# Kernel optimization log

Measured on AMD Instinct MI355X. Metric: run time of the kernel, lower is better.

The kernel has to match this reference:

```python
import jax, jax.numpy as jnp
import numpy as np
import math

B, C, T0, Q0 = 2, 48, 250, 65
H = 192; KS = 4; HS = 1; NH = 4; E = 8; F = 65; DV = 12; HID2 = 384
EPS = 1e-5


def ln_clamp(x, g, b, axes, eps=EPS):
    # LayerNormalization4D / 4DCF: std = sqrt(clamp(var, eps))
    mu = x.mean(axis=axes, keepdims=True)
    var = x.var(axis=axes, keepdims=True)
    return (x - mu) / jnp.sqrt(jnp.maximum(var, eps)) * g + b


def torch_ln(x, g, b, eps=EPS):
    # torch.nn.LayerNorm over last dim: sqrt(var + eps)
    mu = x.mean(axis=-1, keepdims=True)
    var = x.var(axis=-1, keepdims=True)
    return (x - mu) / jnp.sqrt(var + eps) * g + b


def mha(x, in_w, in_b, out_w, out_b, nh):
    # torch.nn.MultiheadAttention, batch_first, self-attention
    N, L, Cm = x.shape
    qkv = x @ in_w.T + in_b
    q, k, v = jnp.split(qkv, 3, axis=-1)
    dh = Cm // nh
    hd = lambda t: t.reshape(N, L, nh, dh).transpose(0, 2, 1, 3)
    q, k, v = hd(q), hd(k), hd(v)
    att = jax.nn.softmax(jnp.einsum('nhld,nhmd->nhlm', q, k) / jnp.sqrt(jnp.float32(dh)), axis=-1)
    o = jnp.einsum('nhlm,nhmd->nhld', att, v).transpose(0, 2, 1, 3).reshape(N, L, Cm)
    return o @ out_w.T + out_b


def lstm_dir(x, wi, wh, bi, bh, reverse=False):
    # x: [N, L, D]; torch gate order i,f,g,o
    Hd = wh.shape[1]
    xs = jnp.swapaxes(x, 0, 1)
    if reverse:
        xs = xs[::-1]
    pre = jnp.einsum('lnd,gd->lng', xs, wi) + bi + bh  # [L,N,4H]

    def step(carry, p):
        hprev, cprev = carry
        gates = p + hprev @ wh.T
        i, f, g, o = jnp.split(gates, 4, axis=-1)
        c = jax.nn.sigmoid(f) * cprev + jax.nn.sigmoid(i) * jnp.tanh(g)
        hnew = jax.nn.sigmoid(o) * jnp.tanh(c)
        return (hnew, c), hnew

    h0 = jnp.zeros((x.shape[0], Hd), x.dtype)
    _, ys = jax.lax.scan(step, (h0, h0), pre)
    if reverse:
        ys = ys[::-1]
    return jnp.swapaxes(ys, 0, 1)


def bilstm(x, wif, whf, bif, bhf, wib, whb, bib, bhb):
    return jnp.concatenate([lstm_dir(x, wif, whf, bif, bhf, False),
                            lstm_dir(x, wib, whb, bib, bhb, True)], axis=-1)


def unfold1d(x, ks, hs):
    # x: [N, C, Q] -> [N, L, C*ks], channel-major like F.unfold
    N, Cc, Qq = x.shape
    L = (Qq - ks) // hs + 1
    cols = jnp.stack([x[:, :, k:k + (L - 1) * hs + 1:hs] for k in range(ks)], axis=-1)  # [N,C,L,ks]
    return cols.transpose(0, 2, 1, 3).reshape(N, L, Cc * ks)


def conv_transpose1d(x, w, b, stride):
    # x: [N, Cin, L], w: [Cin, Cout, ks] (torch ConvTranspose1d layout); overlap-add
    N, Ci, L = x.shape
    ks = w.shape[2]
    out_len = (L - 1) * stride + ks
    y = jnp.einsum('nil,iok->nolk', x, w)
    out = jnp.zeros((N, w.shape[1], out_len), x.dtype)
    for k in range(ks):
        out = out.at[:, :, k:k + (L - 1) * stride + 1:stride].add(y[..., k])
    return out + b[:, None]


def _forward(x, af_in_w, af_in_b, af_out_w, af_out_b, naf_g, naf_b, at_in_w, at_in_b, at_out_w, at_out_b, nat_g, nat_b, intra_ng, intra_nb, inter_ng, inter_nb, intra_wif, intra_whf, intra_bif, intra_bhf, intra_wib, intra_whb, intra_bib, intra_bhb, inter_wif, inter_whf, inter_bif, inter_bhf, inter_wib, inter_whb, inter_bib, inter_bhb, il_w, il_b, itl_w, itl_b, qw, qb, qa, qg, qbt, kw, kb, ka, kg, kbt, vw, vb, va, vg, vbt, pw, pb, pa, pg, pbt, fin_w, fin_b, fdw_w, fdw_b, fout_w, fout_b):
    Bb, Cc, old_T, old_Q = x.shape
    T = math.ceil((old_T - KS) / HS) * HS + KS
    Qd = math.ceil((old_Q - KS) / HS) * HS + KS
    x = jnp.pad(x, ((0, 0), (0, 0), (0, T - old_T), (0, Qd - old_Q)))
    input_ = x

    # ---- intra (frequency) path ----
    z = ln_clamp(input_, intra_ng[None, :, None, None], intra_nb[None, :, None, None], (1,))
    seq = z.transpose(0, 2, 3, 1).reshape(Bb * T, Qd, Cc)  # [B*T, Q, C]
    att = mha(seq, af_in_w, af_in_b, af_out_w, af_out_b, NH)
    seq = torch_ln(att + seq, naf_g, naf_b)
    u = unfold1d(seq.transpose(0, 2, 1), KS, HS)
    r = bilstm(u, intra_wif, intra_whf, intra_bif, intra_bhf, intra_wib, intra_whb, intra_bib, intra_bhb)
    r = conv_transpose1d(r.transpose(0, 2, 1), il_w, il_b, HS)  # [B*T, C, Qd]
    intra = r.reshape(Bb, T, Cc, Qd).transpose(0, 2, 1, 3) + input_
    input_ = intra

    # ---- inter (time) path ----
    z = ln_clamp(input_, inter_ng[None, :, None, None], inter_nb[None, :, None, None], (1,))
    seq = z.transpose(0, 3, 2, 1).reshape(Bb * Qd, T, Cc)  # [B*Q, T, C]
    att = mha(seq, at_in_w, at_in_b, at_out_w, at_out_b, NH)
    seq = torch_ln(att + seq, nat_g, nat_b)
    u = unfold1d(seq.transpose(0, 2, 1), KS, HS)
    r = bilstm(u, inter_wif, inter_whf, inter_bif, inter_bhf, inter_wib, inter_whb, inter_bib, inter_bhb)
    r = conv_transpose1d(r.transpose(0, 2, 1), itl_w, itl_b, HS)  # [B*Qd, C, T]
    inter = r.reshape(Bb, Qd, Cc, T).transpose(0, 2, 3, 1) + input_
    inter = inter[:, :, :old_T, :old_Q]

    # ---- custom per-head conv attention ----
    bt = inter  # [B, C, t, f]

    def head_proj(w, bias, a, g, beta):
        y = jnp.einsum('bctf,hec->hbetf', bt, w) + bias[:, None, :, None, None]
        y = jnp.where(y >= 0, y, a[:, None, None, None, None] * y)  # PReLU per head
        return ln_clamp(y, g[:, None, :, None, :], beta[:, None, :, None, :], (2, 4))

    Qh = head_proj(qw, qb, qa, qg, qbt)  # [h,B,E,t,f]
    Kh = head_proj(kw, kb, ka, kg, kbt)
    Vh = head_proj(vw, vb, va, vg, vbt)  # [h,B,dv,t,f]
    h_, _, E_, t_, f_ = Qh.shape
    dv = Vh.shape[2]
    Qf = Qh.transpose(0, 1, 3, 2, 4).reshape(h_, Bb, t_, E_ * f_)
    Kf = Kh.transpose(0, 1, 3, 2, 4).reshape(h_, Bb, t_, E_ * f_)
    Vf = Vh.transpose(0, 1, 3, 2, 4).reshape(h_, Bb, t_, dv * f_)
    attm = jax.nn.softmax(jnp.einsum('hbtd,hbsd->hbts', Qf, Kf) / jnp.sqrt(jnp.float32(E_ * f_)), axis=-1)
    Vo = jnp.einsum('hbts,hbsd->hbtd', attm, Vf).reshape(h_, Bb, t_, dv, f_)
    Vo = Vo.transpose(1, 0, 3, 2, 4).reshape(Bb, h_ * dv, t_, f_)  # head-major channel concat
    pj = jnp.einsum('bctf,oc->botf', Vo, pw) + pb[None, :, None, None]
    pj = jnp.where(pj >= 0, pj, pa * pj)
    pj = ln_clamp(pj, pg[None, :, None, :], pbt[None, :, None, :], (1, 3))
    out = pj + inter

    # ---- gated-dconv FFN ----
    pi = jnp.einsum('bctf,oc->botf', out, fin_w) + fin_b[None, :, None, None]
    dwc = jax.lax.conv_general_dilated(pi, fdw_w, (1, 1), ((1, 1), (1, 1)),
                                       dimension_numbers=('NCHW', 'OIHW', 'NCHW'),
                                       feature_group_count=fdw_w.shape[0]) + fdw_b[None, :, None, None]
    x1, x2 = jnp.split(dwc, 2, axis=1)
    ffn = jnp.einsum('bctf,oc->botf', jax.nn.gelu(x1, approximate=False) * x2, fout_w) + fout_b[None, :, None, None]
    return ffn + out


def setup_inputs() -> dict:
    key = jax.random.key(0)
    cnt = [0]

    def rn(shape, s=0.05):
        cnt[0] += 1
        return jax.random.normal(jax.random.fold_in(key, cnt[0]), shape, dtype=jnp.float32) * s

    z = lambda *s: jnp.zeros(s, jnp.float32)
    o = lambda *s: jnp.ones(s, jnp.float32)
    d = {}
    d['x'] = rn((B, C, T0, Q0), 1.0)
    for p in ['af', 'at']:
        d[p + '_in_w'] = rn((3 * C, C)); d[p + '_in_b'] = z(3 * C)
        d[p + '_out_w'] = rn((C, C)); d[p + '_out_b'] = z(C)
    d['naf_g'] = o(C); d['naf_b'] = z(C); d['nat_g'] = o(C); d['nat_b'] = z(C)
    d['intra_ng'] = o(C); d['intra_nb'] = z(C); d['inter_ng'] = o(C); d['inter_nb'] = z(C)
    for p in ['intra', 'inter']:
        for s in ['f', 'b']:
            d[p + '_wi' + s] = rn((4 * H, C * KS)); d[p + '_wh' + s] = rn((4 * H, H))
            d[p + '_bi' + s] = z(4 * H); d[p + '_bh' + s] = z(4 * H)
    d['il_w'] = rn((2 * H, C, KS)); d['il_b'] = z(C)
    d['itl_w'] = rn((2 * H, C, KS)); d['itl_b'] = z(C)
    for p, dim in [('q', E), ('k', E), ('v', DV)]:
        d[p + 'w'] = rn((NH, dim, C)); d[p + 'b'] = z(NH, dim)
        d[p + 'a'] = 0.25 * o(NH); d[p + 'g'] = o(NH, dim, F); d[p + 'bt'] = z(NH, dim, F)
    d['pw'] = rn((C, C)); d['pb'] = z(C); d['pa'] = 0.25 * o(1); d['pg'] = o(C, F); d['pbt'] = z(C, F)
    d['fin_w'] = rn((HID2, C)); d['fin_b'] = z(HID2)
    d['fdw_w'] = rn((HID2, 1, 3, 3)); d['fdw_b'] = z(HID2)
    d['fout_w'] = rn((C, HID2 // 2)); d['fout_b'] = z(C)
    return d


def reference(x, af_in_w, af_in_b, af_out_w, af_out_b, naf_g, naf_b, at_in_w, at_in_b, at_out_w, at_out_b, nat_g, nat_b, intra_ng, intra_nb, inter_ng, inter_nb, intra_wif, intra_whf, intra_bif, intra_bhf, intra_wib, intra_whb, intra_bib, intra_bhb, inter_wif, inter_whf, inter_bif, inter_bhf, inter_wib, inter_whb, inter_bib, inter_bhb, il_w, il_b, itl_w, itl_b, qw, qb, qa, qg, qbt, kw, kb, ka, kg, kbt, vw, vb, va, vg, vbt, pw, pb, pa, pg, pbt, fin_w, fin_b, fdw_w, fdw_b, fout_w, fout_b):
    return _forward(x, af_in_w, af_in_b, af_out_w, af_out_b, naf_g, naf_b, at_in_w, at_in_b, at_out_w, at_out_b, nat_g, nat_b, intra_ng, intra_nb, inter_ng, inter_nb, intra_wif, intra_whf, intra_bif, intra_bhf, intra_wib, intra_whb, intra_bib, intra_bhb, inter_wif, inter_whf, inter_bif, inter_bhf, inter_wib, inter_whb, inter_bib, inter_bhb, il_w, il_b, itl_w, itl_b, qw, qb, qa, qg, qbt, kw, kb, ka, kg, kbt, vw, vb, va, vg, vbt, pw, pb, pa, pg, pbt, fin_w, fin_b, fdw_w, fdw_b, fout_w, fout_b)
```

## Files before the change

### kernel.cpp

```cpp
#include <hip/hip_runtime.h>
#include <math.h>

#define EPSV 1e-5f

typedef _Float16 v2h __attribute__((ext_vector_type(2)));

__device__ __forceinline__ float sigf(float x){ return 1.0f/(1.0f+__expf(-x)); }
__device__ __forceinline__ float tanhf_(float x){
  float c = fminf(fmaxf(x,-10.f),10.f);
  float e = __expf(2.0f*c);
  return (e-1.0f)/(e+1.0f);
}

__device__ __forceinline__ float dot2u(unsigned int a, unsigned int b, float c){
#if __has_builtin(__builtin_amdgcn_fdot2)
  v2h av = __builtin_bit_cast(v2h, a);
  v2h bv = __builtin_bit_cast(v2h, b);
  return __builtin_amdgcn_fdot2(av, bv, c, false);
#else
  v2h av = __builtin_bit_cast(v2h, a);
  v2h bv = __builtin_bit_cast(v2h, b);
  return c + (float)av.x*(float)bv.x + (float)av.y*(float)bv.y;
#endif
}
// ... 63 lines not shown
    }
    float inv = 1.0f/den;
    float* outp = att + ((size_t)n*L + r)*48 + h*12;
    for (int d=0; d<12; d++) outp[d] = o[d]*inv;
  }
}

__global__ void k_projres(const float* __restrict__ att, const float* __restrict__ seq,
                          const float* __restrict__ w, const float* __restrict__ bias,
                          float* __restrict__ dst, int NL){
  int i = blockIdx.x*blockDim.x + threadIdx.x;
  if (i >= NL*48) return;
  int o = i % 48; int nl = i/48;
  const float* ar = att + (size_t)nl*48;
  const float* wr = w + o*48;
  float acc = bias[o] + seq[i];
  for (int c=0;c<48;c++) acc += ar[c]*wr[c];
  dst[i] = acc;
}

__global__ void k_rowln(float* __restrict__ buf, const float* __restrict__ g,
                        const float* __restrict__ bb, int NL){
  int nl = blockIdx.x*blockDim.x + threadIdx.x;
  if (nl >= NL) return;
  float* p = buf + (size_t)nl*48;
  float s=0.f, ss=0.f;
  for (int c=0;c<48;c++){ float v=p[c]; s+=v; ss+=v*v; }
  float mu = s*(1.0f/48.0f);
  float var = ss*(1.0f/48.0f) - mu*mu;
  float rs = rsqrtf(var + EPSV);
  for (int c=0;c<48;c++) p[c] = (p[c]-mu)*rs*g[c] + bb[c];
}

__global__ void k_wpack(const float* __restrict__ w, unsigned int* __restrict__ wp){
  int i = blockIdx.x*blockDim.x + threadIdx.x;
  if (i >= 96*768) return;
  int g = i % 768, d2 = i / 768;
  v2h v; v.x = (_Float16)w[g*192 + 2*d2]; v.y = (_Float16)w[g*192 + 2*d2 + 1];
  wp[(size_t)d2*768 + g] = __builtin_bit_cast(unsigned int, v);
}

__global__ void k_wtc(const float* __restrict__ w, float* __restrict__ wt){
  int i = blockIdx.x*blockDim.x + threadIdx.x;
  if (i >= 4*384*48) return;
  int c = i % 48; int ii = (i/48) % 384; int k = i/(48*384);
  wt[i] = w[ii*192 + c*4 + k];
}

__global__ __launch_bounds__(256) void k_pregates(
    const float* __restrict__ seq2, const unsigned int* __restrict__ wi,
    const float* __restrict__ bi, const float* __restrict__ bh,
    _Float16* __restrict__ pre, int L2, int SL){
  __shared__ unsigned int ut[96*16];
  int n = blockIdx.y;
  int l0 = blockIdx.x*16;
  int t = threadIdx.x;
  for (int idx=t; idx<1536; idx+=256){
    int l = idx & 15, d2 = idx >> 4;
    int li = l0 + l;
    int c = d2 >> 1, k0 = (d2 & 1)*2;
    float u0=0.f, u1=0.f;
    if (li < L2){
      const float* p = seq2 + ((size_t)n*SL + li)*48;
      u0 = p[k0*48 + c];
      u1 = p[(k0+1)*48 + c];
    }
    v2h v; v.x=(_Float16)u0; v.y=(_Float16)u1;
    ut[d2*16 + l] = __builtin_bit_cast(unsigned int, v);
  }
  __syncthreads();
  float acc[3][16];
  float b0 = bi[t] + bh[t];
  float b1 = bi[t+256] + bh[t+256];
  float b2 = bi[t+512] + bh[t+512];
  #pragma unroll
  for (int l=0;l<16;l++){ acc[0][l]=b0; acc[1][l]=b1; acc[2][l]=b2; }
  #pragma unroll 4
  for (int d2=0; d2<96; d2++){
    unsigned int w0 = wi[(size_t)d2*768 + t];
    unsigned int w1 = wi[(size_t)d2*768 + t + 256];
    unsigned int w2 = wi[(size_t)d2*768 + t + 512];
    const uint4* u4 = (const uint4*)(ut + d2*16);
    #pragma unroll
    for (int l4=0; l4<4; l4++){
      uint4 uu = u4[l4];
      acc[0][l4*4+0] = dot2u(uu.x, w0, acc[0][l4*4+0]);
      acc[0][l4*4+1] = dot2u(uu.y, w0, acc[0][l4*4+1]);
      acc[0][l4*4+2] = dot2u(uu.z, w0, acc[0][l4*4+2]);
      acc[0][l4*4+3] = dot2u(uu.w, w0, acc[0][l4*4+3]);
      acc[1][l4*4+0] = dot2u(uu.x, w1, acc[1][l4*4+0]);
      acc[1][l4*4+1] = dot2u(uu.y, w1, acc[1][l4*4+1]);
      acc[1][l4*4+2] = dot2u(uu.z, w1, acc[1][l4*4+2]);
      acc[1][l4*4+3] = dot2u(uu.w, w1, acc[1][l4*4+3]);
      acc[2][l4*4+0] = dot2u(uu.x, w2, acc[2][l4*4+0]);
      acc[2][l4*4+1] = dot2u(uu.y, w2, acc[2][l4*4+1]);
      acc[2][l4*4+2] = dot2u(uu.z, w2, acc[2][l4*4+2]);
      acc[2][l4*4+3] = dot2u(uu.w, w2, acc[2][l4*4+3]);
    }
  }
  #pragma unroll
  for (int l=0;l<16;l++){
    int li = l0 + l;
    if (li < L2){
      _Float16* pr = pre + ((size_t)n*L2 + li)*768;
      pr[t]       = (_Float16)acc[0][l];
      pr[t+256]   = (_Float16)acc[1][l];
      pr[t+512]   = (_Float16)acc[2][l];
    }
  }
}

template<int G>
__global__ __launch_bounds__(1024) void k_lstm4(
    const _Float16* __restrict__ pre, _Float16* __restrict__ r,
    const unsigned int* __restrict__ wh_f, const unsigned int* __restrict__ wh_b,
    int N, int L2){
  __shared__ unsigned int hh2[96*G];
  __shared__ float gpart[4*G*768];
  _Float16* hh2h = (_Float16*)hh2;
  int t = threadIdx.x;
  int q = t >> 8, tt = t & 255;
  int dir = blockIdx.y;
  int n0 = blockIdx.x*G;
  const unsigned int* wh = dir ? wh_b : wh_f;
  unsigned int wq[24][3];
  #pragma unroll
  for (int i=0;i<24;i++){
    const unsigned int* wr = wh + (size_t)(q*24+i)*768 + tt;
    wq[i][0] = wr[0]; wq[i][1] = wr[256]; wq[i][2] = wr[512];
  }
  const _Float16* prd = pre + (size_t)dir*(size_t)N*L2*768;
  float cst = 0.f;
  int as = t/192, aj = t - as*192;
  for (int idx=t; idx<96*G; idx+=1024) hh2[idx]=0u;
  __syncthreads();

  for (int step=0; step<L2; step++){
    int l = dir ? (L2-1-step) : step;
    float acc[3][G];
    #pragma unroll
    for (int rr=0;rr<3;rr++)
      #pragma unroll
      for (int s=0;s<G;s++) acc[rr][s]=0.f;
    #pragma unroll
    for (int i=0;i<24;i++){
      unsigned int hhv[G];
      #pragma unroll
      for (int s=0;s<G;s++) hhv[s] = hh2[(q*24+i)*G + s];
      #pragma unroll
      for (int rr=0;rr<3;rr++){
        unsigned int w = wq[i][rr];
        #pragma unroll
        for (int s=0;s<G;s++) acc[rr][s] = dot2u(hhv[s], w, acc[rr][s]);
      }
    }
    #pragma unroll
    for (int rr=0;rr<3;rr++)
      #pragma unroll
      for (int s=0;s<G;s++)
        gpart[(q*G+s)*768 + tt + 256*rr] = acc[rr][s];
    __syncthreads();

    if (t < 192*G){
      int n = n0 + as;
      const _Float16* pp = prd + ((size_t)n*L2 + l)*768;
      float gi = (float)pp[aj];
      float gf = (float)pp[aj+192];
      float gg = (float)pp[aj+384];
      float go = (float)pp[aj+576];
      #pragma unroll
      for (int qq=0; qq<4; qq++){
        const float* gp = gpart + (qq*G+as)*768;
        gi += gp[aj]; gf += gp[aj+192]; gg += gp[aj+384]; go += gp[aj+576];
      }
      float ig = sigf(gi), fg = sigf(gf), g2 = tanhf_(gg), og = sigf(go);
      cst = fg*cst + ig*g2;
      float hn = og*tanhf_(cst);
      r[((size_t)n*L2 + l)*384 + dir*192 + aj] = (_Float16)hn;
      hh2h[((aj>>1)*G + as)*2 + (aj&1)] = (_Float16)hn;
    }
    __syncthreads();
  }
}

__global__ __launch_bounds__(256) void k_convt2(
    const _Float16* __restrict__ r, const float* __restrict__ wt2,
    const float* __restrict__ bias, const float* __restrict__ resid,
    float* __restrict__ dst, int L2, int OL, int mode){
  __shared__ float wsh[384*48];
  int n = blockIdx.y;
  int p0 = blockIdx.x*64;
  int tid = threadIdx.x;
  int pos = p0 + (tid >> 2);
  int cq = tid & 3;
  float4 acc[3];
  acc[0] = make_float4(0,0,0,0); acc[1] = make_float4(0,0,0,0); acc[2] = make_float4(0,0,0,0);

  for (int k=0; k<4; k++){
    const float4* wk4 = (const float4*)(wt2 + (size_t)k*384*48);
    float4* wsh4 = (float4*)wsh;
    for (int i=tid; i<4608; i+=256) wsh4[i] = wk4[i];
    __syncthreads();
    int l = pos - k;
    if (l >= 0 && l < L2){
      const uint2* rr2 = (const uint2*)(r + ((size_t)n*L2 + l)*384);
      const float4* wb = (const float4*)(wsh + cq*12);
      #pragma unroll 4
      for (int ii4=0; ii4<96; ii4++){
        uint2 rp = rr2[ii4];
        v2h p0h = __builtin_bit_cast(v2h, rp.x);
        v2h p1h = __builtin_bit_cast(v2h, rp.y);
        float4 rv = make_float4((float)p0h.x, (float)p0h.y, (float)p1h.x, (float)p1h.y);
        const float4* w0 = wb + (ii4*4)*12;
        float4 wa, wbv, wc;
        wa = w0[0]; wbv = w0[1]; wc = w0[2];
        acc[0].x += rv.x*wa.x; acc[0].y += rv.x*wa.y; acc[0].z += rv.x*wa.z; acc[0].w += rv.x*wa.w;
        acc[1].x += rv.x*wbv.x; acc[1].y += rv.x*wbv.y; acc[1].z += rv.x*wbv.z; acc[1].w += rv.x*wbv.w;
        acc[2].x += rv.x*wc.x; acc[2].y += rv.x*wc.y; acc[2].z += rv.x*wc.z; acc[2].w += rv.x*wc.w;
        wa = w0[12]; wbv = w0[13]; wc = w0[14];
        acc[0].x += rv.y*wa.x; acc[0].y += rv.y*wa.y; acc[0].z += rv.y*wa.z; acc[0].w += rv.y*wa.w;
        acc[1].x += rv.y*wbv.x; acc[1].y += rv.y*wbv.y; acc[1].z += rv.y*wbv.z; acc[1].w += rv.y*wbv.w;
        acc[2].x += rv.y*wc.x; acc[2].y += rv.y*wc.y; acc[2].z += rv.y*wc.z; acc[2].w += rv.y*wc.w;
        wa = w0[24]; wbv = w0[25]; wc = w0[26];
        acc[0].x += rv.z*wa.x; acc[0].y += rv.z*wa.y; acc[0].z += rv.z*wa.z; acc[0].w += rv.z*wa.w;
        acc[1].x += rv.z*wbv.x; acc[1].y += rv.z*wbv.y; acc[1].z += rv.z*wbv.z; acc[1].w += rv.z*wbv.w;
        acc[2].x += rv.z*wc.x; acc[2].y += rv.z*wc.y; acc[2].z += rv.z*wc.z; acc[2].w += rv.z*wc.w;
        wa = w0[36]; wbv = w0[37]; wc = w0[38];
        acc[0].x += rv.w*wa.x; acc[0].y += rv.w*wa.y; acc[0].z += rv.w*wa.z; acc[0].w += rv.w*wa.w;
        acc[1].x += rv.w*wbv.x; acc[1].y += rv.w*wbv.y; acc[1].z += rv.w*wbv.z; acc[1].w += rv.w*wbv.w;
        acc[2].x += rv.w*wc.x; acc[2].y += rv.w*wc.y; acc[2].z += rv.w*wc.z; acc[2].w += rv.w*wc.w;
      }
    }
    __syncthreads();
  }

  if (pos < OL){
    float a[12];
    a[0]=acc[0].x; a[1]=acc[0].y; a[2]=acc[0].z; a[3]=acc[0].w;
    a[4]=acc[1].x; a[5]=acc[1].y; a[6]=acc[1].z; a[7]=acc[1].w;
    a[8]=acc[2].x; a[9]=acc[2].y; a[10]=acc[2].z; a[11]=acc[2].w;
    for (int c12=0; c12<12; c12++){
      int c = cq*12 + c12;
      size_t oidx;
      if (mode==0){ int b = n/250, t = n%250; oidx = (((size_t)b*48+c)*250+t)*65 + pos; }
      else        { int b = n/65,  q = n%65;  oidx = (((size_t)b*48+c)*250+pos)*65 + q; }
      dst[oidx] = a[c12] + bias[c] + resid[oidx];
    }
  }
}

__global__ void k_headproj(const float* __restrict__ bt, const float* __restrict__ w,
                           const float* __restrict__ bias, const float* __restrict__ alpha,
                           float* __restrict__ dst, int dim){
  int i = blockIdx.x*blockDim.x + threadIdx.x;
  int total = 4*2*250*dim*65;
  if (i >= total) return;
  int f = i % 65;
  int e = (i/65) % dim;
  int t = (i/(65*dim)) % 250;
  int b = (i/(65*dim*250)) % 2;
  int h = i/(65*dim*250*2);
  const float* wr = w + (h*dim+e)*48;
  const float* bp = bt + (size_t)b*48*250*65 + (size_t)t*65 + f;
  float acc = bias[h*dim+e];
  for (int c=0;c<48;c++) acc += bp[(size_t)c*250*65]*wr[c];
  if (acc < 0.f) acc *= alpha[h];
  dst[i] = acc;
}

__global__ void k_headln(float* __restrict__ buf, const float* __restrict__ g,
                         const float* __restrict__ bt_, int dim){
  __shared__ float r1[256];
  __shared__ float r2[256];
  int bx = blockIdx.x;
  int h = bx/500;
  int n = dim*65;
  float* p = buf + (size_t)bx*n;
  const float* gp = g + h*n;
  const float* bp = bt_ + h*n;
  float s=0.f, ss=0.f;
  for (int k=threadIdx.x; k<n; k+=256){ float v=p[k]; s+=v; ss+=v*v; }
  r1[threadIdx.x]=s; r2[threadIdx.x]=ss; __syncthreads();
  for (int st=128; st>0; st>>=1){
    if (threadIdx.x < st){ r1[threadIdx.x]+=r1[threadIdx.x+st]; r2[threadIdx.x]+=r2[threadIdx.x+st]; }
    __syncthreads();
  }
  float mu = r1[0]/(float)n, var = r2[0]/(float)n - mu*mu;
  float rs = rsqrtf(fmaxf(var, EPSV));
  for (int k=threadIdx.x; k<n; k+=256) p[k] = (p[k]-mu)*rs*gp[k] + bp[k];
}

__global__ void k_ktrans(const float* __restrict__ Kh, float* __restrict__ KT){
  int i = blockIdx.x*blockDim.x + threadIdx.x;
  if (i >= 8*520*250) return;
  int s2 = i % 250;
  int d  = (i/250) % 520;
  int hb = i/(250*520);
  KT[i] = Kh[((size_t)hb*250 + s2)*520 + d];
}

__global__ __launch_bounds__(256) void k_headattn2(
    const float* __restrict__ Qp, const float* __restrict__ KT,
    const float* __restrict__ Vp, float* __restrict__ Vo){
  __shared__ float qsh[10*520];
  __shared__ float psh[10*250];
  __shared__ float rinv[10];
  int t0 = blockIdx.x*10;
  int hb = blockIdx.y;
  int h = hb >> 1, b = hb & 1;
  int tid = threadIdx.x;
  const float* qbase = Qp + ((size_t)hb*250 + t0)*520;
  for (int i=tid; i<5200; i+=256) qsh[i] = qbase[i];
  __syncthreads();
  const float scale = 0.04385290096535147f;
  if (tid < 250){
    float sc[10];
    #pragma unroll
    for (int i=0;i<10;i++) sc[i]=0.f;
    const float* kcol = KT + (size_t)hb*520*250 + tid;
    for (int d=0; d<520; d++){
      float kv = kcol[(size_t)d*250];
      #pragma unroll
      for (int i=0;i<10;i++) sc[i] += qsh[i*520+d]*kv;
    }
    #pragma unroll
    for (int i=0;i<10;i++) psh[i*250+tid] = sc[i]*scale;
  }
  __syncthreads();
  if (tid < 10){
    float m = -1e30f;
    for (int s2=0;s2<250;s2++) m = fmaxf(m, psh[tid*250+s2]);
// ... 54 lines not shown
  if (acc < 0.f) acc *= pa[0];
  pj[i] = acc;
}

__global__ void k_pln(const float* __restrict__ pj, const float* __restrict__ pg,
                      const float* __restrict__ pbt, const float* __restrict__ inter,
                      float* __restrict__ outb){
  __shared__ float r1[256];
  __shared__ float r2[256];
  int bx = blockIdx.x;
  int t = bx % 250, b = bx/250;
  const float* base = pj + (size_t)b*48*250*65 + (size_t)t*65;
  float s=0.f, ss=0.f;
  for (int k=threadIdx.x; k<3120; k+=256){
    int c = k/65, f = k%65;
    float v = base[(size_t)c*250*65 + f];
    s+=v; ss+=v*v;
  }
  r1[threadIdx.x]=s; r2[threadIdx.x]=ss; __syncthreads();
  for (int st=128; st>0; st>>=1){
    if (threadIdx.x<st){ r1[threadIdx.x]+=r1[threadIdx.x+st]; r2[threadIdx.x]+=r2[threadIdx.x+st]; }
    __syncthreads();
  }
  float mu = r1[0]*(1.0f/3120.0f), var = r2[0]*(1.0f/3120.0f) - mu*mu;
  float rs = rsqrtf(fmaxf(var, EPSV));
  for (int k=threadIdx.x; k<3120; k+=256){
    int c = k/65, f = k%65;
    size_t idx = (((size_t)b*48+c)*250 + t)*65 + f;
    float v = pj[idx];
    outb[idx] = (v-mu)*rs*pg[c*65+f] + pbt[c*65+f] + inter[idx];
  }
}

__global__ void k_fin(const float* __restrict__ outb, const float* __restrict__ w,
                      const float* __restrict__ bias, float* __restrict__ pi){
  int i = blockIdx.x*blockDim.x + threadIdx.x;
  if (i >= 2*384*250*65) return;
  int f = i % 65;
  int t = (i/65) % 250;
  int o = (i/(65*250)) % 384;
  int b = i/(65*250*384);
  const float* xp = outb + (size_t)b*48*250*65 + (size_t)t*65 + f;
  const float* wr = w + o*48;
  float acc = bias[o];
  for (int c=0;c<48;c++) acc += xp[(size_t)c*250*65]*wr[c];
  pi[i] = acc;
}

__global__ void k_dwg(const float* __restrict__ pi, const float* __restrict__ dw,
                      const float* __restrict__ db, float* __restrict__ gbuf){
  int i = blockIdx.x*blockDim.x + threadIdx.x;
  if (i >= 2*192*250*65) return;
  int f = i % 65;
  int t = (i/65) % 250;
  int j = (i/(65*250)) % 192;
  int b = i/(65*250*192);
  float x12[2];
  for (int half=0; half<2; half++){
    int ch = j + half*192;
    const float* base = pi + ((size_t)b*384 + ch)*250*65;
    const float* wr = dw + ch*9;
    float acc = db[ch];
    for (int dt=-1; dt<=1; dt++){
      int tt = t+dt;
      if (tt<0||tt>=250) continue;
      for (int df=-1; df<=1; df++){
        int ff = f+df;
        if (ff<0||ff>=65) continue;
        acc += base[(size_t)tt*65+ff]*wr[(dt+1)*3 + (df+1)];
      }
    }
    x12[half]=acc;
  }
  float x1 = x12[0];
  float g = 0.5f*x1*(1.0f+erff(x1*0.70710678118654752f));
  gbuf[i] = g * x12[1];
}

__global__ void k_final(const float* __restrict__ gbuf, const float* __restrict__ w,
                        const float* __restrict__ bias, const float* __restrict__ outb,
                        float* __restrict__ dout){
  int i = blockIdx.x*blockDim.x + threadIdx.x;
  if (i >= 2*48*250*65) return;
  int f = i % 65;
  int t = (i/65) % 250;
  int o = (i/(65*250)) % 48;
  int b = i/(65*250*48);
  const float* gp = gbuf + (size_t)b*192*250*65 + (size_t)t*65 + f;
  const float* wr = w + o*192;
  float acc = bias[o];
  for (int j=0;j<192;j++) acc += gp[(size_t)j*250*65]*wr[j];
  dout[i] = acc + outb[i];
}

extern "C" void kernel_launch(void* const* d_in, const int* in_sizes, int n_in,
                              void* d_out, int out_size, void* d_ws, size_t ws_size,
                              hipStream_t stream) {
  (void)in_sizes; (void)n_in; (void)out_size; (void)ws_size;
  auto in = [&](int i){ return (const float*)d_in[i]; };
  const float* x        = in(0);
  const float* af_in_w  = in(1);  const float* af_in_b  = in(2);
  const float* af_out_w = in(3);  const float* af_out_b = in(4);
  const float* at_in_w  = in(5);  const float* at_in_b  = in(6);
  const float* at_out_w = in(7);  const float* at_out_b = in(8);
  const float* naf_g = in(9),  *naf_b = in(10), *nat_g = in(11), *nat_b = in(12);
  const float* intra_ng = in(13), *intra_nb = in(14), *inter_ng = in(15), *inter_nb = in(16);
  const float* intra_wif = in(17), *intra_whf = in(18), *intra_bif = in(19), *intra_bhf = in(20);
  const float* intra_wib = in(21), *intra_whb = in(22), *intra_bib = in(23), *intra_bhb = in(24);
  const float* inter_wif = in(25), *inter_whf = in(26), *inter_bif = in(27), *inter_bhf = in(28);
  const float* inter_wib = in(29), *inter_whb = in(30), *inter_bib = in(31), *inter_bhb = in(32);
  const float* il_w = in(33), *il_b = in(34), *itl_w = in(35), *itl_b = in(36);
  const float* qw = in(37), *qb = in(38), *qa = in(39), *qg = in(40), *qbt = in(41);
  const float* kw = in(42), *kb = in(43), *ka = in(44), *kg = in(45), *kbt = in(46);
  const float* vw = in(47), *vb = in(48), *va = in(49), *vg = in(50), *vbt = in(51);
  const float* pw = in(52), *pb = in(53), *pa = in(54), *pg = in(55), *pbt = in(56);
  const float* fin_w = in(57), *fin_b = in(58), *fdw_w = in(59), *fdw_b = in(60);
  const float* fout_w = in(61), *fout_b = in(62);

  float* ws = (float*)d_ws;
  float* buf_intra = ws + 0;
  float* buf_bt    = ws + 1560000;
  float* buf_out   = ws + 3120000;
  unsigned int* wpk = (unsigned int*)(ws + 4680000);
  float* wtc       = ws + 5269824;
  float* scr       = ws + 5417280;
  float* s_seq2 = scr;
  float* s_seq  = scr + 1560000;
  float* s_qkv  = scr + 3120000;
  float* s_att  = scr + 7800000;
  _Float16* s_pre = (_Float16*)(scr + 1560000);
  _Float16* s_r   = (_Float16*)(scr + 26220480);
  float* s_Qh = scr;
  float* s_Kh = scr + 1040000;
  float* s_Vh = scr + 2080000;
  float* s_Vo = scr + 3640000;
  float* s_pj = scr + 5200000;
  float* s_KT = scr + 6760000;
  float* s_pi = scr;
  float* s_g  = scr + 12480000;

  const int thr = 256;
  auto cdiv = [](int a, int b){ return (a+b-1)/b; };

  k_wpack<<<cdiv(73728,thr),thr,0,stream>>>(intra_wif, wpk + 0*73728);
  k_wpack<<<cdiv(73728,thr),thr,0,stream>>>(intra_whf, wpk + 1*73728);
  k_wpack<<<cdiv(73728,thr),thr,0,stream>>>(intra_wib, wpk + 2*73728);
  k_wpack<<<cdiv(73728,thr),thr,0,stream>>>(intra_whb, wpk + 3*73728);
  k_wpack<<<cdiv(73728,thr),thr,0,stream>>>(inter_wif, wpk + 4*73728);
  k_wpack<<<cdiv(73728,thr),thr,0,stream>>>(inter_whf, wpk + 5*73728);
  k_wpack<<<cdiv(73728,thr),thr,0,stream>>>(inter_wib, wpk + 6*73728);
  k_wpack<<<cdiv(73728,thr),thr,0,stream>>>(inter_whb, wpk + 7*73728);
  k_wtc<<<cdiv(73728,thr),thr,0,stream>>>(il_w,  wtc + 0*73728);
  k_wtc<<<cdiv(73728,thr),thr,0,stream>>>(itl_w, wtc + 1*73728);

  k_ln_chan<<<cdiv(2*250*65,thr), thr, 0, stream>>>(x, s_seq, intra_ng, intra_nb, 0);
  k_qkv<<<cdiv(500*65*144,thr), thr, 0, stream>>>(s_seq, af_in_w, af_in_b, s_qkv, 500*65);
  k_mha<<<dim3(500,4), 256, 0, stream>>>(s_qkv, s_att, 500, 65);
  k_projres<<<cdiv(500*65*48,thr), thr, 0, stream>>>(s_att, s_seq, af_out_w, af_out_b, s_seq2, 500*65);
  k_rowln<<<cdiv(32500,thr), thr, 0, stream>>>(s_seq2, naf_g, naf_b, 32500);
  {
    const size_t dstr = (size_t)500*62*768;
    k_pregates<<<dim3(4,500), 256, 0, stream>>>(s_seq2, wpk+0*73728, intra_bif, intra_bhf, s_pre,        62, 65);
    k_pregates<<<dim3(4,500), 256, 0, stream>>>(s_seq2, wpk+2*73728, intra_bib, intra_bhb, s_pre + dstr, 62, 65);
  }
  k_lstm4<4><<<dim3(125,2), 1024, 0, stream>>>(s_pre, s_r, wpk+1*73728, wpk+3*73728, 500, 62);
  k_convt2<<<dim3(2,500), 256, 0, stream>>>(s_r, wtc+0*73728, il_b, x, buf_intra, 62, 65, 0);

  k_ln_chan<<<cdiv(2*250*65,thr),thr,0,stream>>>(buf_intra, s_seq, inter_ng, inter_nb, 1);
  k_qkv<<<cdiv(130*250*144,thr),thr,0,stream>>>(s_seq, at_in_w, at_in_b, s_qkv, 130*250);
  k_mha<<<dim3(130,4), 256, 0, stream>>>(s_qkv, s_att, 130, 250);
  k_projres<<<cdiv(130*250*48,thr),thr,0,stream>>>(s_att, s_seq, at_out_w, at_out_b, s_seq2, 130*250);
  k_rowln<<<cdiv(32500,thr),thr,0,stream>>>(s_seq2, nat_g, nat_b, 32500);
  {
    const size_t dstr = (size_t)130*247*768;
    k_pregates<<<dim3(16,130), 256, 0, stream>>>(s_seq2, wpk+4*73728, inter_bif, inter_bhf, s_pre,        247, 250);
    k_pregates<<<dim3(16,130), 256, 0, stream>>>(s_seq2, wpk+6*73728, inter_bib, inter_bhb, s_pre + dstr, 247, 250);
  }
  k_lstm4<2><<<dim3(65,2), 1024, 0, stream>>>(s_pre, s_r, wpk+5*73728, wpk+7*73728, 130, 247);
  k_convt2<<<dim3(4,130), 256, 0, stream>>>(s_r, wtc+1*73728, itl_b, buf_intra, buf_bt, 247, 250, 1);

  k_headproj<<<cdiv(4*2*250*8*65,thr),thr,0,stream>>>(buf_bt, qw, qb, qa, s_Qh, 8);
  k_headln<<<2000,256,0,stream>>>(s_Qh, qg, qbt, 8);
  k_headproj<<<cdiv(4*2*250*8*65,thr),thr,0,stream>>>(buf_bt, kw, kb, ka, s_Kh, 8);
  k_headln<<<2000,256,0,stream>>>(s_Kh, kg, kbt, 8);
  k_headproj<<<cdiv(4*2*250*12*65,thr),thr,0,stream>>>(buf_bt, vw, vb, va, s_Vh, 12);
  k_headln<<<2000,256,0,stream>>>(s_Vh, vg, vbt, 12);
  k_ktrans<<<cdiv(8*520*250,thr),thr,0,stream>>>(s_Kh, s_KT);
  k_headattn2<<<dim3(25,8), 256, 0, stream>>>(s_Qh, s_KT, s_Vh, s_Vo);
  k_pproj<<<cdiv(2*48*250*65,thr),thr,0,stream>>>(s_Vo, pw, pb, pa, s_pj);
  k_pln<<<500,256,0,stream>>>(s_pj, pg, pbt, buf_bt, buf_out);

  k_fin<<<cdiv(2*384*250*65,thr),thr,0,stream>>>(buf_out, fin_w, fin_b, s_pi);
  k_dwg<<<cdiv(2*192*250*65,thr),thr,0,stream>>>(s_pi, fdw_w, fdw_b, s_g);
  k_final<<<cdiv(2*48*250*65,thr),thr,0,stream>>>(s_g, fout_w, fout_b, buf_out, (float*)d_out);
}
```

Before: 2.813 ms.

## Fuse weight prep, head proj+LN, transpose LSTM output, and regroup LSTM/conv kernels

Merges the ten weight-packing launches into one kernel. Fuses the head projection with its LayerNorm and writes K directly in transposed layout, which drops the separate k_ktrans pass. The LSTM kernel now prefetches its pre-gate values before the recurrent matmul, reads hidden state with vector LDS loads, and writes a transposed fp16-pair output. The LSTM also uses smaller sequence groups (more blocks) to raise occupancy. The transposed-conv kernel reads that layout with fdot2 and no longer stages weights in LDS, and the final 1x1 convs compute four output channels per thread to reuse input loads.

```diff
diff --git a/kernel.cpp b/kernel.cpp
--- a/kernel.cpp
+++ b/kernel.cpp
@@ -119,19 +119,29 @@
   for (int c=0;c<48;c++) p[c] = (p[c]-mu)*rs*g[c] + bb[c];
 }
 
-__global__ void k_wpack(const float* __restrict__ w, unsigned int* __restrict__ wp){
-  int i = blockIdx.x*blockDim.x + threadIdx.x;
-  if (i >= 96*768) return;
-  int g = i % 768, d2 = i / 768;
-  v2h v; v.x = (_Float16)w[g*192 + 2*d2]; v.y = (_Float16)w[g*192 + 2*d2 + 1];
-  wp[(size_t)d2*768 + g] = __builtin_bit_cast(unsigned int, v);
-}
-
-__global__ void k_wtc(const float* __restrict__ w, float* __restrict__ wt){
-  int i = blockIdx.x*blockDim.x + threadIdx.x;
-  if (i >= 4*384*48) return;
-  int c = i % 48; int ii = (i/48) % 384; int k = i/(48*384);
-  wt[i] = w[ii*192 + c*4 + k];
+__global__ void k_prep(const float* __restrict__ s0, const float* __restrict__ s1,
+                       const float* __restrict__ s2, const float* __restrict__ s3,
+                       const float* __restrict__ s4, const float* __restrict__ s5,
+                       const float* __restrict__ s6, const float* __restrict__ s7,
+                       const float* __restrict__ c0, const float* __restrict__ c1,
+                       unsigned int* __restrict__ wpk, unsigned int* __restrict__ wtp){
+  int i = blockIdx.x*blockDim.x + threadIdx.x;
+  if (i < 589824){
+    int seg = i/73728, off = i - seg*73728;
+    const float* w = (seg==0)?s0:(seg==1)?s1:(seg==2)?s2:(seg==3)?s3:(seg==4)?s4:(seg==5)?s5:(seg==6)?s6:s7;
+    int g = off % 768, d2 = off / 768;
+    v2h v; v.x = (_Float16)w[g*192 + 2*d2]; v.y = (_Float16)w[g*192 + 2*d2 + 1];
+    wpk[(size_t)seg*73728 + (size_t)d2*768 + g] = __builtin_bit_cast(unsigned int, v);
+  } else if (i < 589824 + 2*36864){
+    int j = i - 589824;
+    int seg = j/36864, off = j - seg*36864;
+    const float* w = seg ? c1 : c0;
+    int c = off % 48; int ii2 = (off/48) % 192; int k = off/(48*192);
+    v2h v;
+    v.x = (_Float16)w[(2*ii2)*192 + c*4 + k];
+    v.y = (_Float16)w[(2*ii2+1)*192 + c*4 + k];
+    wtp[(size_t)seg*36864 + off] = __builtin_bit_cast(unsigned int, v);
+  }
 }
 
 __global__ __launch_bounds__(256) void k_pregates(
@@ -198,8 +208,8 @@
 }
 
 template<int G>
-__global__ __launch_bounds__(1024) void k_lstm4(
-    const _Float16* __restrict__ pre, _Float16* __restrict__ r,
+__global__ __launch_bounds__(1024) void k_lstm5(
+    const _Float16* __restrict__ pre, unsigned int* __restrict__ rT2,
     const unsigned int* __restrict__ wh_f, const unsigned int* __restrict__ wh_b,
     int N, int L2){
   __shared__ unsigned int hh2[96*G];
@@ -219,42 +229,55 @@
   const _Float16* prd = pre + (size_t)dir*(size_t)N*L2*768;
   float cst = 0.f;
   int as = t/192, aj = t - as*192;
+  bool actv = (t < 192*G);
+  const unsigned short* pbase = (const unsigned short*)prd;
+  if (actv) pbase = (const unsigned short*)(prd + ((size_t)(n0+as)*L2)*768) + aj;
   for (int idx=t; idx<96*G; idx+=1024) hh2[idx]=0u;
   __syncthreads();
 
   for (int step=0; step<L2; step++){
     int l = dir ? (L2-1-step) : step;
-    float acc[3][G];
-    #pragma unroll
-    for (int rr=0;rr<3;rr++)
-      #pragma unroll
-      for (int s=0;s<G;s++) acc[rr][s]=0.f;
+    unsigned short p0=0,p1=0,p2=0,p3=0;
+    if (actv){
+      const unsigned short* pp = pbase + (size_t)l*768;
+      p0 = pp[0]; p1 = pp[192]; p2 = pp[384]; p3 = pp[576];
+    }
+    float acc0[G], acc1[G], acc2[G];
+    #pragma unroll
+    for (int s=0;s<G;s++){ acc0[s]=0.f; acc1[s]=0.f; acc2[s]=0.f; }
     #pragma unroll
     for (int i=0;i<24;i++){
       unsigned int hhv[G];
+      if (G==4){
+        uint4 hv = ((const uint4*)hh2)[q*24+i];
+        hhv[0]=hv.x; hhv[1]=hv.y; hhv[2]=hv.z; hhv[3]=hv.w;
+      } else if (G==2){
+        uint2 hv = ((const uint2*)hh2)[q*24+i];
+        hhv[0]=hv.x; hhv[1]=hv.y;
+      } else {
+        hhv[0] = hh2[q*24+i];
+      }
+      unsigned int w0 = wq[i][0], w1 = wq[i][1], w2 = wq[i][2];
       #pragma unroll
-      for (int s=0;s<G;s++) hhv[s] = hh2[(q*24+i)*G + s];
-      #pragma unroll
-      for (int rr=0;rr<3;rr++){
-        unsigned int w = wq[i][rr];
-        #pragma unroll
-        for (int s=0;s<G;s++) acc[rr][s] = dot2u(hhv[s], w, acc[rr][s]);
+      for (int s=0;s<G;s++){
+        acc0[s] = dot2u(hhv[s], w0, acc0[s]);
+        acc1[s] = dot2u(hhv[s], w1, acc1[s]);
+        acc2[s] = dot2u(hhv[s], w2, acc2[s]);
       }
     }
     #pragma unroll
-    for (int rr=0;rr<3;rr++)
-      #pragma unroll
-      for (int s=0;s<G;s++)
-        gpart[(q*G+s)*768 + tt + 256*rr] = acc[rr][s];
+    for (int s=0;s<G;s++){
+      gpart[(q*G+s)*768 + tt]       = acc0[s];
+      gpart[(q*G+s)*768 + tt + 256] = acc1[s];
+      gpart[(q*G+s)*768 + tt + 512] = acc2[s];
+    }
     __syncthreads();
 
-    if (t < 192*G){
-      int n = n0 + as;
-      const _Float16* pp = prd + ((size_t)n*L2 + l)*768;
-      float gi = (float)pp[aj];
-      float gf = (float)pp[aj+192];
-      float gg = (float)pp[aj+384];
-      float go = (float)pp[aj+576];
+    if (actv){
+      float gi = (float)__builtin_bit_cast(_Float16, p0);
+      float gf = (float)__builtin_bit_cast(_Float16, p1);
+      float gg = (float)__builtin_bit_cast(_Float16, p2);
+      float go = (float)__builtin_bit_cast(_Float16, p3);
       #pragma unroll
       for (int qq=0; qq<4; qq++){
         const float* gp = gpart + (qq*G+as)*768;
@@ -263,127 +286,88 @@
       float ig = sigf(gi), fg = sigf(gf), g2 = tanhf_(gg), og = sigf(go);
       cst = fg*cst + ig*g2;
       float hn = og*tanhf_(cst);
-      r[((size_t)n*L2 + l)*384 + dir*192 + aj] = (_Float16)hn;
       hh2h[((aj>>1)*G + as)*2 + (aj&1)] = (_Float16)hn;
     }
     __syncthreads();
-  }
-}
-
-__global__ __launch_bounds__(256) void k_convt2(
-    const _Float16* __restrict__ r, const float* __restrict__ wt2,
+
+    if (t < 96*G){
+      int s = t/96, ii2 = t - s*96;
+      unsigned int v = hh2[ii2*G + s];
+      rT2[((size_t)(n0+s)*192 + dir*96 + ii2)*L2 + l] = v;
+    }
+  }
+}
+
+__global__ __launch_bounds__(256) void k_convt4(
+    const unsigned int* __restrict__ rT2, const unsigned int* __restrict__ wtp,
     const float* __restrict__ bias, const float* __restrict__ resid,
     float* __restrict__ dst, int L2, int OL, int mode){
-  __shared__ float wsh[384*48];
   int n = blockIdx.y;
-  int p0 = blockIdx.x*64;
-  int tid = threadIdx.x;
-  int pos = p0 + (tid >> 2);
-  int cq = tid & 3;
-  float4 acc[3];
-  acc[0] = make_float4(0,0,0,0); acc[1] = make_float4(0,0,0,0); acc[2] = make_float4(0,0,0,0);
-
-  for (int k=0; k<4; k++){
-    const float4* wk4 = (const float4*)(wt2 + (size_t)k*384*48);
-    float4* wsh4 = (float4*)wsh;
-    for (int i=tid; i<4608; i+=256) wsh4[i] = wk4[i];
-    __syncthreads();
+  int pos = blockIdx.x*64 + (threadIdx.x & 63);
+  int cq = __builtin_amdgcn_readfirstlane((int)(threadIdx.x >> 6));
+  float acc[12];
+  #pragma unroll
+  for (int c=0;c<12;c++) acc[c]=0.f;
+  const unsigned int* rbase = rT2 + (size_t)n*192*L2;
+  for (int k=0;k<4;k++){
     int l = pos - k;
-    if (l >= 0 && l < L2){
-      const uint2* rr2 = (const uint2*)(r + ((size_t)n*L2 + l)*384);
-      const float4* wb = (const float4*)(wsh + cq*12);
-      #pragma unroll 4
-      for (int ii4=0; ii4<96; ii4++){
-        uint2 rp = rr2[ii4];
-        v2h p0h = __builtin_bit_cast(v2h, rp.x);
-        v2h p1h = __builtin_bit_cast(v2h, rp.y);
-        float4 rv = make_float4((float)p0h.x, (float)p0h.y, (float)p1h.x, (float)p1h.y);
-        const float4* w0 = wb + (ii4*4)*12;
-        float4 wa, wbv, wc;
-        wa = w0[0]; wbv = w0[1]; wc = w0[2];
-        acc[0].x += rv.x*wa.x; acc[0].y += rv.x*wa.y; acc[0].z += rv.x*wa.z; acc[0].w += rv.x*wa.w;
-        acc[1].x += rv.x*wbv.x; acc[1].y += rv.x*wbv.y; acc[1].z += rv.x*wbv.z; acc[1].w += rv.x*wbv.w;
-        acc[2].x += rv.x*wc.x; acc[2].y += rv.x*wc.y; acc[2].z += rv.x*wc.z; acc[2].w += rv.x*wc.w;
-        wa = w0[12]; wbv = w0[13]; wc = w0[14];
-        acc[0].x += rv.y*wa.x; acc[0].y += rv.y*wa.y; acc[0].z += rv.y*wa.z; acc[0].w += rv.y*wa.w;
-        acc[1].x += rv.y*wbv.x; acc[1].y += rv.y*wbv.y; acc[1].z += rv.y*wbv.z; acc[1].w += rv.y*wbv.w;
-        acc[2].x += rv.y*wc.x; acc[2].y += rv.y*wc.y; acc[2].z += rv.y*wc.z; acc[2].w += rv.y*wc.w;
-        wa = w0[24]; wbv = w0[25]; wc = w0[26];
-        acc[0].x += rv.z*wa.x; acc[0].y += rv.z*wa.y; acc[0].z += rv.z*wa.z; acc[0].w += rv.z*wa.w;
-        acc[1].x += rv.z*wbv.x; acc[1].y += rv.z*wbv.y; acc[1].z += rv.z*wbv.z; acc[1].w += rv.z*wbv.w;
-        acc[2].x += rv.z*wc.x; acc[2].y += rv.z*wc.y; acc[2].z += rv.z*wc.z; acc[2].w += rv.z*wc.w;
-        wa = w0[36]; wbv = w0[37]; wc = w0[38];
-        acc[0].x += rv.w*wa.x; acc[0].y += rv.w*wa.y; acc[0].z += rv.w*wa.z; acc[0].w += rv.w*wa.w;
-        acc[1].x += rv.w*wbv.x; acc[1].y += rv.w*wbv.y; acc[1].z += rv.w*wbv.z; acc[1].w += rv.w*wbv.w;
-        acc[2].x += rv.w*wc.x; acc[2].y += rv.w*wc.y; acc[2].z += rv.w*wc.z; acc[2].w += rv.w*wc.w;
-      }
-    }
-    __syncthreads();
-  }
-
+    bool v = (l>=0) && (l<L2);
+    int lc = v ? l : 0;
+    const unsigned int* wk = wtp + (size_t)k*192*48 + cq*12;
+    #pragma unroll 4
+    for (int ii2=0; ii2<192; ii2++){
+      unsigned int rp = v ? rbase[(size_t)ii2*L2 + lc] : 0u;
+      const unsigned int* wrow = wk + ii2*48;
+      #pragma unroll
+      for (int c=0;c<12;c++) acc[c] = dot2u(rp, wrow[c], acc[c]);
+    }
+  }
   if (pos < OL){
-    float a[12];
-    a[0]=acc[0].x; a[1]=acc[0].y; a[2]=acc[0].z; a[3]=acc[0].w;
-    a[4]=acc[1].x; a[5]=acc[1].y; a[6]=acc[1].z; a[7]=acc[1].w;
-    a[8]=acc[2].x; a[9]=acc[2].y; a[10]=acc[2].z; a[11]=acc[2].w;
-    for (int c12=0; c12<12; c12++){
+    for (int c12=0;c12<12;c12++){
       int c = cq*12 + c12;
       size_t oidx;
-      if (mode==0){ int b = n/250, t = n%250; oidx = (((size_t)b*48+c)*250+t)*65 + pos; }
-      else        { int b = n/65,  q = n%65;  oidx = (((size_t)b*48+c)*250+pos)*65 + q; }
-      dst[oidx] = a[c12] + bias[c] + resid[oidx];
-    }
-  }
-}
-
-__global__ void k_headproj(const float* __restrict__ bt, const float* __restrict__ w,
-                           const float* __restrict__ bias, const float* __restrict__ alpha,
-                           float* __restrict__ dst, int dim){
-  int i = blockIdx.x*blockDim.x + threadIdx.x;
-  int total = 4*2*250*dim*65;
-  if (i >= total) return;
-  int f = i % 65;
-  int e = (i/65) % dim;
-  int t = (i/(65*dim)) % 250;
-  int b = (i/(65*dim*250)) % 2;
-  int h = i/(65*dim*250*2);
-  const float* wr = w + (h*dim+e)*48;
-  const float* bp = bt + (size_t)b*48*250*65 + (size_t)t*65 + f;
-  float acc = bias[h*dim+e];
-  for (int c=0;c<48;c++) acc += bp[(size_t)c*250*65]*wr[c];
-  if (acc < 0.f) acc *= alpha[h];
-  dst[i] = acc;
-}
-
-__global__ void k_headln(float* __restrict__ buf, const float* __restrict__ g,
-                         const float* __restrict__ bt_, int dim){
+      if (mode==0){ int b=n/250, t=n%250; oidx = (((size_t)b*48+c)*250+t)*65+pos; }
+      else        { int b=n/65,  qq=n%65; oidx = (((size_t)b*48+c)*250+pos)*65+qq; }
+      dst[oidx] = acc[c12] + bias[c] + resid[oidx];
+    }
+  }
+}
+
+__global__ __launch_bounds__(256) void k_hproj(
+    const float* __restrict__ bt, const float* __restrict__ w,
+    const float* __restrict__ bias, const float* __restrict__ alpha,
+    const float* __restrict__ g, const float* __restrict__ beta,
+    float* __restrict__ dst, int dim, int kt_mode){
+  __shared__ float ybuf[780];
   __shared__ float r1[256];
   __shared__ float r2[256];
   int bx = blockIdx.x;
-  int h = bx/500;
-  int n = dim*65;
-  float* p = buf + (size_t)bx*n;
-  const float* gp = g + h*n;
-  const float* bp = bt_ + h*n;
+  int h = bx/500; int rem = bx - h*500; int b = rem/250; int t = rem - b*250;
+  int ny = dim*65;
+  int tid = threadIdx.x;
+  const float* bbase = bt + (size_t)b*48*250*65 + (size_t)t*65;
+  float al = alpha[h];
   float s=0.f, ss=0.f;
-  for (int k=threadIdx.x; k<n; k+=256){ float v=p[k]; s+=v; ss+=v*v; }
-  r1[threadIdx.x]=s; r2[threadIdx.x]=ss; __syncthreads();
+  for (int kidx=tid; kidx<ny; kidx+=256){
+    int e = kidx/65, f = kidx - e*65;
+    const float* wr = w + (h*dim+e)*48;
+    float acc = bias[h*dim+e];
+    for (int c=0;c<48;c++) acc += bbase[(size_t)c*250*65 + f]*wr[c];
+    if (acc < 0.f) acc *= al;
+    ybuf[kidx] = acc; s += acc; ss += acc*acc;
+  }
+  r1[tid]=s; r2[tid]=ss; __syncthreads();
   for (int st=128; st>0; st>>=1){
-    if (threadIdx.x < st){ r1[threadIdx.x]+=r1[threadIdx.x+st]; r2[threadIdx.x]+=r2[threadIdx.x+st]; }
+    if (tid<st){ r1[tid]+=r1[tid+st]; r2[tid]+=r2[tid+st]; }
     __syncthreads();
   }
-  float mu = r1[0]/(float)n, var = r2[0]/(float)n - mu*mu;
+  float mu = r1[0]/(float)ny, var = r2[0]/(float)ny - mu*mu;
   float rs = rsqrtf(fmaxf(var, EPSV));
-  for (int k=threadIdx.x; k<n; k+=256) p[k] = (p[k]-mu)*rs*gp[k] + bp[k];
-}
-
-__global__ void k_ktrans(const float* __restrict__ Kh, float* __restrict__ KT){
-  int i = blockIdx.x*blockDim.x + threadIdx.x;
-  if (i >= 8*520*250) return;
-  int s2 = i % 250;
-  int d  = (i/250) % 520;
-  int hb = i/(250*520);
-  KT[i] = Kh[((size_t)hb*250 + s2)*520 + d];
+  for (int kidx=tid; kidx<ny; kidx+=256){
+    float y = (ybuf[kidx]-mu)*rs*g[h*ny+kidx] + beta[h*ny+kidx];
+    if (kt_mode) dst[((size_t)(h*2+b)*520 + kidx)*250 + t] = y;
+    else         dst[(size_t)bx*ny + kidx] = y;
+  }
 }
 
 __global__ __launch_bounds__(256) void k_headattn2(
@@ -504,19 +488,23 @@
   }
 }
 
-__global__ void k_fin(const float* __restrict__ outb, const float* __restrict__ w,
-                      const float* __restrict__ bias, float* __restrict__ pi){
-  int i = blockIdx.x*blockDim.x + threadIdx.x;
-  if (i >= 2*384*250*65) return;
+__global__ void k_fin2(const float* __restrict__ outb, const float* __restrict__ w,
+                       const float* __restrict__ bias, float* __restrict__ pi){
+  int i = blockIdx.x*blockDim.x + threadIdx.x;
+  if (i >= 2*96*250*65) return;
   int f = i % 65;
   int t = (i/65) % 250;
-  int o = (i/(65*250)) % 384;
-  int b = i/(65*250*384);
+  int og = (i/(65*250)) % 96;
+  int b = i/(65*250*96);
   const float* xp = outb + (size_t)b*48*250*65 + (size_t)t*65 + f;
-  const float* wr = w + o*48;
-  float acc = bias[o];
-  for (int c=0;c<48;c++) acc += xp[(size_t)c*250*65]*wr[c];
-  pi[i] = acc;
+  const float* w0 = w + og*4*48;
+  float a0=bias[og*4], a1=bias[og*4+1], a2=bias[og*4+2], a3=bias[og*4+3];
+  for (int c=0;c<48;c++){
+    float xv = xp[(size_t)c*250*65];
+    a0 += xv*w0[c]; a1 += xv*w0[48+c]; a2 += xv*w0[96+c]; a3 += xv*w0[144+c];
+  }
+  size_t o0 = (((size_t)b*384 + og*4)*250 + t)*65 + f;
+  pi[o0] = a0; pi[o0+16250] = a1; pi[o0+2*16250] = a2; pi[o0+3*16250] = a3;
 }
 
 __global__ void k_dwg(const float* __restrict__ pi, const float* __restrict__ dw,
@@ -549,20 +537,27 @@
   gbuf[i] = g * x12[1];
 }
 
-__global__ void k_final(const float* __restrict__ gbuf, const float* __restrict__ w,
-                        const float* __restrict__ bias, const float* __restrict__ outb,
-                        float* __restrict__ dout){
-  int i = blockIdx.x*blockDim.x + threadIdx.x;
-  if (i >= 2*48*250*65) return;
+__global__ void k_final2(const float* __restrict__ gbuf, const float* __restrict__ w,
+                         const float* __restrict__ bias, const float* __restrict__ outb,
+                         float* __restrict__ dout){
+  int i = blockIdx.x*blockDim.x + threadIdx.x;
+  if (i >= 2*12*250*65) return;
   int f = i % 65;
   int t = (i/65) % 250;
-  int o = (i/(65*250)) % 48;
-  int b = i/(65*250*48);
+  int og = (i/(65*250)) % 12;
+  int b = i/(65*250*12);
   const float* gp = gbuf + (size_t)b*192*250*65 + (size_t)t*65 + f;
-  const float* wr = w + o*192;
-  float acc = bias[o];
-  for (int j=0;j<192;j++) acc += gp[(size_t)j*250*65]*wr[j];
-  dout[i] = acc + outb[i];
+  const float* w0 = w + og*4*192;
+  float a0=bias[og*4], a1=bias[og*4+1], a2=bias[og*4+2], a3=bias[og*4+3];
+  for (int j=0;j<192;j++){
+    float gv = gp[(size_t)j*250*65];
+    a0 += gv*w0[j]; a1 += gv*w0[192+j]; a2 += gv*w0[384+j]; a3 += gv*w0[576+j];
+  }
+  size_t o0 = (((size_t)b*48 + og*4)*250 + t)*65 + f;
+  dout[o0]         = a0 + outb[o0];
+  dout[o0+16250]   = a1 + outb[o0+16250];
+  dout[o0+2*16250] = a2 + outb[o0+2*16250];
+  dout[o0+3*16250] = a3 + outb[o0+3*16250];
 }
 
 extern "C" void kernel_launch(void* const* d_in, const int* in_sizes, int n_in,
@@ -594,36 +589,29 @@
   float* buf_bt    = ws + 1560000;
   float* buf_out   = ws + 3120000;
   unsigned int* wpk = (unsigned int*)(ws + 4680000);
-  float* wtc       = ws + 5269824;
-  float* scr       = ws + 5417280;
+  unsigned int* wtp = (unsigned int*)(ws + 5269824);
+  float* scr       = ws + 5343552;
   float* s_seq2 = scr;
   float* s_seq  = scr + 1560000;
   float* s_qkv  = scr + 3120000;
   float* s_att  = scr + 7800000;
   _Float16* s_pre = (_Float16*)(scr + 1560000);
-  _Float16* s_r   = (_Float16*)(scr + 26220480);
+  unsigned int* s_rT2 = (unsigned int*)(scr + 26220480);
   float* s_Qh = scr;
-  float* s_Kh = scr + 1040000;
+  float* s_KT = scr + 1040000;
   float* s_Vh = scr + 2080000;
   float* s_Vo = scr + 3640000;
   float* s_pj = scr + 5200000;
-  float* s_KT = scr + 6760000;
   float* s_pi = scr;
   float* s_g  = scr + 12480000;
 
   const int thr = 256;
   auto cdiv = [](int a, int b){ return (a+b-1)/b; };
 
-  k_wpack<<<cdiv(73728,thr),thr,0,stream>>>(intra_wif, wpk + 0*73728);
-  k_wpack<<<cdiv(73728,thr),thr,0,stream>>>(intra_whf, wpk + 1*73728);
-  k_wpack<<<cdiv(73728,thr),thr,0,stream>>>(intra_wib, wpk + 2*73728);
-  k_wpack<<<cdiv(73728,thr),thr,0,stream>>>(intra_whb, wpk + 3*73728);
-  k_wpack<<<cdiv(73728,thr),thr,0,stream>>>(inter_wif, wpk + 4*73728);
-  k_wpack<<<cdiv(73728,thr),thr,0,stream>>>(inter_whf, wpk + 5*73728);
-  k_wpack<<<cdiv(73728,thr),thr,0,stream>>>(inter_wib, wpk + 6*73728);
-  k_wpack<<<cdiv(73728,thr),thr,0,stream>>>(inter_whb, wpk + 7*73728);
-  k_wtc<<<cdiv(73728,thr),thr,0,stream>>>(il_w,  wtc + 0*73728);
-  k_wtc<<<cdiv(73728,thr),thr,0,stream>>>(itl_w, wtc + 1*73728);
+  k_prep<<<cdiv(663552,thr),thr,0,stream>>>(
+      intra_wif, intra_whf, intra_wib, intra_whb,
+      inter_wif, inter_whf, inter_wib, inter_whb,
+      il_w, itl_w, wpk, wtp);
 
   k_ln_chan<<<cdiv(2*250*65,thr), thr, 0, stream>>>(x, s_seq, intra_ng, intra_nb, 0);
   k_qkv<<<cdiv(500*65*144,thr), thr, 0, stream>>>(s_seq, af_in_w, af_in_b, s_qkv, 500*65);
@@ -635,8 +623,8 @@
     k_pregates<<<dim3(4,500), 256, 0, stream>>>(s_seq2, wpk+0*73728, intra_bif, intra_bhf, s_pre,        62, 65);
     k_pregates<<<dim3(4,500), 256, 0, stream>>>(s_seq2, wpk+2*73728, intra_bib, intra_bhb, s_pre + dstr, 62, 65);
   }
-  k_lstm4<4><<<dim3(125,2), 1024, 0, stream>>>(s_pre, s_r, wpk+1*73728, wpk+3*73728, 500, 62);
-  k_convt2<<<dim3(2,500), 256, 0, stream>>>(s_r, wtc+0*73728, il_b, x, buf_intra, 62, 65, 0);
+  k_lstm5<2><<<dim3(250,2), 1024, 0, stream>>>(s_pre, s_rT2, wpk+1*73728, wpk+3*73728, 500, 62);
+  k_convt4<<<dim3(2,500), 256, 0, stream>>>(s_rT2, wtp+0*36864, il_b, x, buf_intra, 62, 65, 0);
 
   k_ln_chan<<<cdiv(2*250*65,thr),thr,0,stream>>>(buf_intra, s_seq, inter_ng, inter_nb, 1);
   k_qkv<<<cdiv(130*250*144,thr),thr,0,stream>>>(s_seq, at_in_w, at_in_b, s_qkv, 130*250);
@@ -648,21 +636,17 @@
     k_pregates<<<dim3(16,130), 256, 0, stream>>>(s_seq2, wpk+4*73728, inter_bif, inter_bhf, s_pre,        247, 250);
     k_pregates<<<dim3(16,130), 256, 0, stream>>>(s_seq2, wpk+6*73728, inter_bib, inter_bhb, s_pre + dstr, 247, 250);
   }
-  k_lstm4<2><<<dim3(65,2), 1024, 0, stream>>>(s_pre, s_r, wpk+5*73728, wpk+7*73728, 130, 247);
-  k_convt2<<<dim3(4,130), 256, 0, stream>>>(s_r, wtc+1*73728, itl_b, buf_intra, buf_bt, 247, 250, 1);
-
-  k_headproj<<<cdiv(4*2*250*8*65,thr),thr,0,stream>>>(buf_bt, qw, qb, qa, s_Qh, 8);
-  k_headln<<<2000,256,0,stream>>>(s_Qh, qg, qbt, 8);
-  k_headproj<<<cdiv(4*2*250*8*65,thr),thr,0,stream>>>(buf_bt, kw, kb, ka, s_Kh, 8);
-  k_headln<<<2000,256,0,stream>>>(s_Kh, kg, kbt, 8);
-  k_headproj<<<cdiv(4*2*250*12*65,thr),thr,0,stream>>>(buf_bt, vw, vb, va, s_Vh, 12);
-  k_headln<<<2000,256,0,stream>>>(s_Vh, vg, vbt, 12);
-  k_ktrans<<<cdiv(8*520*250,thr),thr,0,stream>>>(s_Kh, s_KT);
+  k_lstm5<1><<<dim3(130,2), 1024, 0, stream>>>(s_pre, s_rT2, wpk+5*73728, wpk+7*73728, 130, 247);
+  k_convt4<<<dim3(4,130), 256, 0, stream>>>(s_rT2, wtp+1*36864, itl_b, buf_intra, buf_bt, 247, 250, 1);
+
+  k_hproj<<<2000,256,0,stream>>>(buf_bt, qw, qb, qa, qg, qbt, s_Qh, 8, 0);
+  k_hproj<<<2000,256,0,stream>>>(buf_bt, kw, kb, ka, kg, kbt, s_KT, 8, 1);
+  k_hproj<<<2000,256,0,stream>>>(buf_bt, vw, vb, va, vg, vbt, s_Vh, 12, 0);
   k_headattn2<<<dim3(25,8), 256, 0, stream>>>(s_Qh, s_KT, s_Vh, s_Vo);
   k_pproj<<<cdiv(2*48*250*65,thr),thr,0,stream>>>(s_Vo, pw, pb, pa, s_pj);
   k_pln<<<500,256,0,stream>>>(s_pj, pg, pbt, buf_bt, buf_out);
 
-  k_fin<<<cdiv(2*384*250*65,thr),thr,0,stream>>>(buf_out, fin_w, fin_b, s_pi);
+  k_fin2<<<cdiv(2*96*250*65,thr),thr,0,stream>>>(buf_out, fin_w, fin_b, s_pi);
   k_dwg<<<cdiv(2*192*250*65,thr),thr,0,stream>>>(s_pi, fdw_w, fdw_b, s_g);
-  k_final<<<cdiv(2*48*250*65,thr),thr,0,stream>>>(s_g, fout_w, fout_b, buf_out, (float*)d_out);
-}
+  k_final2<<<cdiv(2*12*250*65,thr),thr,0,stream>>>(s_g, fout_w, fout_b, buf_out, (float*)d_out);
+}
```

Measured after the change: 2.562 ms. 1.1x faster.
